# Performance work log

Hardware: AMD Instinct MI355X
Metric: run time of the kernel (lower is better)

## Reference

```python
import jax, jax.numpy as jnp
import numpy as np

B, L, D, H = 2, 2048, 1024, 16
hd = D // H
SCALE = hd ** -0.5
K = 3


def _dwconv(x_bcl, w, b):
    # x_bcl: [B, C, L]; w: [C, 1, K] depthwise; b: [C]
    y = jax.lax.conv_general_dilated(
        x_bcl, w, window_strides=(1,), padding=[((K - 1) // 2, (K - 1) // 2)],
        feature_group_count=x_bcl.shape[1],
        dimension_numbers=('NCH', 'OIH', 'NCH'))
    return y + b[None, :, None]


def setup_inputs() -> dict:
    key = jax.random.key(0)
    ks = jax.random.split(key, 11)
    def n(k, shape, s=0.02):
        return jax.random.normal(k, shape, dtype=jnp.float32) * s
    return {
        'x': jax.random.normal(ks[0], (B, L, D), dtype=jnp.float32),
        'wq': n(ks[1], (D, D)), 'wk': n(ks[2], (D, D)),
        'wv': n(ks[3], (D, D)), 'wo': n(ks[4], (D, D)),
        'cq_w': n(ks[5], (D, 1, K), 0.3), 'cq_b': n(ks[6], (D,)),
        'ck_w': n(ks[7], (D, 1, K), 0.3), 'ck_b': n(ks[8], (D,)),
        'cv_w': n(ks[9], (D, 1, K), 0.3), 'cv_b': n(ks[10], (D,)),
    }


def reference(x, wq, wk, wv, wo, cq_w, cq_b, ck_w, ck_b, cv_w, cv_b):
    # Linear projections (torch Linear: y = x @ W^T); note k scaled BEFORE conv
    q = jnp.einsum('bld,ed->ble', x, wq)
    k = jnp.einsum('bld,ed->ble', x, wk) * SCALE
    v = jnp.einsum('bld,ed->ble', x, wv)
    # Depthwise conv along sequence dim
    q = _dwconv(q.transpose(0, 2, 1), cq_w, cq_b).transpose(0, 2, 1)
    k = _dwconv(k.transpose(0, 2, 1), ck_w, ck_b).transpose(0, 2, 1)
    v = _dwconv(v.transpose(0, 2, 1), cv_w, cv_b).transpose(0, 2, 1)
    # Split heads -> [B, H, L, hd]
    q = q.reshape(B, L, H, hd).transpose(0, 2, 1, 3)
    k = k.reshape(B, L, H, hd).transpose(0, 2, 1, 3)
    v = v.reshape(B, L, H, hd).transpose(0, 2, 1, 3)
    sim = jnp.einsum('bhqd,bhkd->bhqk', q, k)
    causal = jnp.triu(jnp.ones((L, L), dtype=bool), k=1)
    sim = jnp.where(causal[None, None], -jnp.inf, sim)
    attn = jax.nn.softmax(sim, axis=-1)
    ctxt = jnp.einsum('bhqk,bhkd->bhqd', attn, v)
    out = ctxt.transpose(0, 2, 1, 3).reshape(B, L, D)
    out = jnp.einsum('bld,ed->ble', out, wo)
    return out, attn
```

## Files before the change

kernel.cpp:

```cpp
#include <hip/hip_runtime.h>
#include <hip/hip_bf16.h>


constexpr int B = 2, L = 2048, D = 1024, H = 16, HD = 64;
constexpr float SCALE = 0.125f;
constexpr int M_ROWS = B * L;

typedef short sh8 __attribute__((ext_vector_type(8)));
typedef float f32x4 __attribute__((ext_vector_type(4)));

__device__ __forceinline__ unsigned short f2bf(float f) {
  union { float f; unsigned u; } x; x.f = f;
  unsigned r = x.u + 0x7FFFu + ((x.u >> 16) & 1u);
  return (unsigned short)(r >> 16);
}
__device__ __forceinline__ float bf2f(unsigned short u) {
  union { unsigned u; float f; } x; x.u = ((unsigned)u) << 16;
  return x.f;
}

#define GLL16(gsrc, ldsbase)                                                  \
  __builtin_amdgcn_global_load_lds(                                           \
      (const __attribute__((address_space(1))) void*)(gsrc),                  \
      (__attribute__((address_space(3))) void*)(ldsbase), 16, 0, 0)

__global__ __launch_bounds__(256) void cast_x_bf16(const float* __restrict__ in,
                                                   unsigned short* __restrict__ out) {
  const size_t g = (size_t)blockIdx.x * 256 + threadIdx.x;
  const float4 a = *(const float4*)&in[g * 8];
  const float4 b = *(const float4*)&in[g * 8 + 4];
  ushort4 o0, o1;
  o0.x = f2bf(a.x); o0.y = f2bf(a.y); o0.z = f2bf(a.z); o0.w = f2bf(a.w);
  o1.x = f2bf(b.x); o1.y = f2bf(b.y); o1.z = f2bf(b.z); o1.w = f2bf(b.w);
  *(ushort4*)&out[g * 8] = o0;
  *(ushort4*)&out[g * 8 + 4] = o1;
}

__global__ __launch_bounds__(256) void cast_w4_bf16(
    const float* __restrict__ wq, const float* __restrict__ wk,
    const float* __restrict__ wv, const float* __restrict__ wo,
    unsigned short* __restrict__ out) {
  const int z = blockIdx.z;
  const float* src = (z == 0) ? wq : (z == 1) ? wk : (z == 2) ? wv : wo;
  unsigned short* dst = out + (size_t)z * 1024 * 1024;
  const size_t g = (size_t)blockIdx.x * 256 + threadIdx.x;
  const float4 a = *(const float4*)&src[g * 8];
  const float4 b = *(const float4*)&src[g * 8 + 4];
  ushort4 o0, o1;
  o0.x = f2bf(a.x); o0.y = f2bf(a.y); o0.z = f2bf(a.z); o0.w = f2bf(a.w);
  o1.x = f2bf(b.x); o1.y = f2bf(b.y); o1.z = f2bf(b.z); o1.w = f2bf(b.w);
  *(ushort4*)&dst[g * 8] = o0;
  *(ushort4*)&dst[g * 8 + 4] = o1;
}

template <bool BF16OUT>
__device__ __forceinline__ void gemm_lds_body(
    const unsigned short* __restrict__ A, const unsigned short* __restrict__ W,
    void* __restrict__ Y, float alpha) {
  __shared__ __align__(16) unsigned short As[128 * 64];
  __shared__ __align__(16) unsigned short Ws[128 * 64];
  const int tid = threadIdx.x;
  const int wave = tid >> 6, lane = tid & 63;
  const int m = lane & 15, kg = lane >> 4;
  const int m0 = blockIdx.y * 128, n0 = blockIdx.x * 128;
  const int wr = wave >> 1, wc = wave & 1;
  const int srow = lane >> 3;
  const int schunk = lane & 7;

  f32x4 acc[4][4];
#pragma unroll
  for (int i = 0; i < 4; ++i)
#pragma unroll
    for (int j = 0; j < 4; ++j) acc[i][j] = (f32x4){0.f, 0.f, 0.f, 0.f};

  for (int k0 = 0; k0 < 1024; k0 += 64) {
#pragma unroll
    for (int c = 0; c < 4; ++c) {
      const int grp = wave * 4 + c;
      const int row = grp * 8 + srow;
      GLL16(A + (size_t)(m0 + row) * 1024 + k0 + schunk * 8,
            (char*)As + grp * 1024);
      GLL16(W + (size_t)(n0 + row) * 1024 + k0 + schunk * 8,
            (char*)Ws + grp * 1024);
    }
    __syncthreads();
    sh8 af[4][2], bfr[4][2];
#pragma unroll
    for (int i = 0; i < 4; ++i)
#pragma unroll
      for (int s = 0; s < 2; ++s) {
        af[i][s] = *(const sh8*)&As[(wr * 64 + i * 16 + m) * 64 + s * 32 + kg * 8];
        bfr[i][s] = *(const sh8*)&Ws[(wc * 64 + i * 16 + m) * 64 + s * 32 + kg * 8];
      }
#pragma unroll
    for (int s = 0; s < 2; ++s)
#pragma unroll
      for (int i = 0; i < 4; ++i)
#pragma unroll
        for (int j = 0; j < 4; ++j)
          acc[i][j] = __builtin_amdgcn_mfma_f32_16x16x32_bf16(af[i][s], bfr[j][s],
                                                             acc[i][j], 0, 0, 0);
    __syncthreads();
  }

  const int R = m0 + wr * 64, C = n0 + wc * 64;
#pragma unroll
  for (int i = 0; i < 4; ++i)
#pragma unroll
    for (int j = 0; j < 4; ++j)
#pragma unroll
      for (int reg = 0; reg < 4; ++reg) {
        const int row = R + i * 16 + kg * 4 + reg;
        const int col = C + j * 16 + m;
        const float v = acc[i][j][reg] * alpha;
        if constexpr (BF16OUT)
          ((unsigned short*)Y)[(size_t)row * 1024 + col] = f2bf(v);
        else
          ((float*)Y)[(size_t)row * 1024 + col] = v;
      }
}

__global__ __launch_bounds__(256) void proj_mfma(
    const unsigned short* __restrict__ xb, const unsigned short* __restrict__ wb4,
    unsigned short* __restrict__ qpre, unsigned short* __restrict__ kpre,
    unsigned short* __restrict__ vpre) {
  const int z = blockIdx.z;
  const unsigned short* W = wb4 + (size_t)z * 1024 * 1024;
  unsigned short* Yo = (z == 0) ? qpre : (z == 1) ? kpre : vpre;
  gemm_lds_body<true>(xb, W, Yo, (z == 1) ? SCALE : 1.0f);
}

__global__ __launch_bounds__(256) void outproj_mfma(
    const unsigned short* __restrict__ ctxtb, const unsigned short* __restrict__ wob,
    float* __restrict__ out) {
  gemm_lds_body<false>(ctxtb, wob, out, 1.0f);
}

__global__ __launch_bounds__(256) void dwconv_bf16(const unsigned short* __restrict__ in,
                                                   const float* __restrict__ w,
                                                   const float* __restrict__ bias,
                                                   unsigned short* __restrict__ out) {
  const int gid = blockIdx.x * 256 + threadIdx.x;
  const int d4 = gid % (D / 4);
  const int l = (gid / (D / 4)) % L;
  const int b = gid / ((D / 4) * L);
  const int d = d4 * 4;
  const size_t base = ((size_t)b * L + l) * D + d;
  const ushort4 cu = *(const ushort4*)&in[base];
  ushort4 pu = make_ushort4(0, 0, 0, 0), nu = make_ushort4(0, 0, 0, 0);
  if (l > 0) pu = *(const ushort4*)&in[base - D];
  if (l < L - 1) nu = *(const ushort4*)&in[base + D];
  float o0 = w[(d + 0) * 3 + 0] * bf2f(pu.x) + w[(d + 0) * 3 + 1] * bf2f(cu.x) + w[(d + 0) * 3 + 2] * bf2f(nu.x) + bias[d + 0];
  float o1 = w[(d + 1) * 3 + 0] * bf2f(pu.y) + w[(d + 1) * 3 + 1] * bf2f(cu.y) + w[(d + 1) * 3 + 2] * bf2f(nu.y) + bias[d + 1];
  float o2 = w[(d + 2) * 3 + 0] * bf2f(pu.z) + w[(d + 2) * 3 + 1] * bf2f(cu.z) + w[(d + 2) * 3 + 2] * bf2f(nu.z) + bias[d + 2];
  float o3 = w[(d + 3) * 3 + 0] * bf2f(pu.w) + w[(d + 3) * 3 + 1] * bf2f(cu.w) + w[(d + 3) * 3 + 2] * bf2f(nu.w) + bias[d + 3];
  ushort4 o;
  o.x = f2bf(o0); o.y = f2bf(o1); o.z = f2bf(o2); o.w = f2bf(o3);
  *(ushort4*)&out[base] = o;
}

__global__ __launch_bounds__(256) void dwconv_v_t(const unsigned short* __restrict__ in,
                                                  const float* __restrict__ w,
                                                  const float* __restrict__ bias,
                                                  unsigned short* __restrict__ vt) {
  const int l0 = blockIdx.x * 64;
  const int h = blockIdx.y, b = blockIdx.z;
  const int d0 = h * HD;
  __shared__ unsigned short T[64][72];
  const int tid = threadIdx.x;
  const int dq = (tid & 15) * 4, lr = tid >> 4;
#pragma unroll
  for (int pass = 0; pass < 4; ++pass) {
    const int l = l0 + pass * 16 + lr;
    const size_t base = ((size_t)b * L + l) * D + d0 + dq;
    const ushort4 cu = *(const ushort4*)&in[base];
    ushort4 pu = make_ushort4(0, 0, 0, 0), nu = make_ushort4(0, 0, 0, 0);
    if (l > 0) pu = *(const ushort4*)&in[base - D];
    if (l < L - 1) nu = *(const ushort4*)&in[base + D];
    const float c[4] = {bf2f(cu.x), bf2f(cu.y), bf2f(cu.z), bf2f(cu.w)};
    const float pp[4] = {bf2f(pu.x), bf2f(pu.y), bf2f(pu.z), bf2f(pu.w)};
    const float nn[4] = {bf2f(nu.x), bf2f(nu.y), bf2f(nu.z), bf2f(nu.w)};
#pragma unroll
    for (int j = 0; j < 4; ++j) {
      const int d = d0 + dq + j;
      float o = w[d * 3 + 0] * pp[j] + w[d * 3 + 1] * c[j] + w[d * 3 + 2] * nn[j] + bias[d];
      T[dq + j][pass * 16 + lr] = f2bf(o);
    }
  }
  __syncthreads();
  const int dd = tid >> 2, lq = (tid & 3) * 16;
  const size_t rbase = ((size_t)(b * H + h) * HD + dd) * L + l0 + lq;
#pragma unroll
  for (int i = 0; i < 16; i += 4) {
    ushort4 o;
    o.x = T[dd][lq + i + 0]; o.y = T[dd][lq + i + 1];
    o.z = T[dd][lq + i + 2]; o.w = T[dd][lq + i + 3];
    *(ushort4*)&vt[rbase + i] = o;
  }
}

__global__ __launch_bounds__(256) void flash_pv(
    const unsigned short* __restrict__ qb, const unsigned short* __restrict__ kb,
    const unsigned short* __restrict__ vt, float* __restrict__ linv_g,
    unsigned short* __restrict__ ctxtb) {
  const int p = blockIdx.x, h = blockIdx.y, b = blockIdx.z;
  const int tid = threadIdx.x;
  const int wave = tid >> 6, lane = tid & 63;
  const int m = lane & 15, kg = lane >> 4;

  __shared__ unsigned short P_sh[4][16 * 72];

  const size_t bh = (size_t)b * H + h;
  const unsigned short* qbase = qb + (size_t)b * L * D + h * HD;
  const unsigned short* kbase = kb + (size_t)b * L * D + h * HD;
  const unsigned short* vbase = vt + bh * HD * L;
  float* lbase = linv_g + bh * L;

  for (int which = 0; which < 2; ++which) {
    const int qt = which ? (31 - p) : p;
    const int q0 = qt * 64;
    const int r0 = q0 + wave * 16;
    const int crow = kg * 4;

    sh8 qf[2];
#pragma unroll
    for (int s = 0; s < 2; ++s)
      qf[s] = *(const sh8*)(qbase + (size_t)(r0 + m) * D + s * 32 + kg * 8);

    f32x4 cacc[4];
#pragma unroll
    for (int ct = 0; ct < 4; ++ct) cacc[ct] = (f32x4){0.f, 0.f, 0.f, 0.f};
    float lsum[4] = {0.f, 0.f, 0.f, 0.f};

    for (int kt = 0; kt <= qt; ++kt) {
      const int kcol0 = kt * 64;
#pragma unroll
      for (int ct = 0; ct < 4; ++ct) {
        f32x4 sacc = {0.f, 0.f, 0.f, 0.f};
#pragma unroll
        for (int s = 0; s < 2; ++s) {
          sh8 kf = *(const sh8*)(kbase + (size_t)(kcol0 + ct * 16 + m) * D + s * 32 + kg * 8);
          sacc = __builtin_amdgcn_mfma_f32_16x16x32_bf16(qf[s], kf, sacc, 0, 0, 0);
        }
        const int col = kcol0 + ct * 16 + m;
#pragma unroll
        for (int reg = 0; reg < 4; ++reg) {
          const int row = r0 + crow + reg;
          const float e = (col <= row) ? __expf(sacc[reg]) : 0.f;
          lsum[reg] += e;
          P_sh[wave][(crow + reg) * 72 + ct * 16 + m] = f2bf(e);
        }
      }
      sh8 pf[2];
#pragma unroll
      for (int s = 0; s < 2; ++s)
        pf[s] = *(const sh8*)&P_sh[wave][m * 72 + s * 32 + kg * 8];
#pragma unroll
      for (int ct = 0; ct < 4; ++ct) {
#pragma unroll
        for (int s = 0; s < 2; ++s) {
          sh8 vf = *(const sh8*)(vbase + (size_t)(ct * 16 + m) * L + kcol0 + s * 32 + kg * 8);
          cacc[ct] = __builtin_amdgcn_mfma_f32_16x16x32_bf16(pf[s], vf, cacc[ct], 0, 0, 0);
        }
      }
    }

    float linv[4];
#pragma unroll
    for (int reg = 0; reg < 4; ++reg) {
      float v = lsum[reg];
      v += __shfl_xor(v, 1); v += __shfl_xor(v, 2);
      v += __shfl_xor(v, 4); v += __shfl_xor(v, 8);
      linv[reg] = 1.0f / v;
    }

#pragma unroll
    for (int ct = 0; ct < 4; ++ct)
#pragma unroll
      for (int reg = 0; reg < 4; ++reg)
        ctxtb[(size_t)(b * L + r0 + crow + reg) * D + h * HD + ct * 16 + m] =
            f2bf(cacc[ct][reg] * linv[reg]);

    if (m == 0) {
#pragma unroll
      for (int reg = 0; reg < 4; ++reg) lbase[r0 + crow + reg] = linv[reg];
    }
  }
}

__global__ __launch_bounds__(256) void attn_write(
    const unsigned short* __restrict__ qb, const unsigned short* __restrict__ kb,
    const float* __restrict__ linv_g, float* __restrict__ attn) {
  const int tc = blockIdx.x, tr = blockIdx.y, bhz = blockIdx.z;
  const int b = bhz >> 4, h = bhz & 15;
  float* attnb = attn + (size_t)bhz * L * L;

  if (tc > tr) {
    const int t = threadIdx.x;
    const int r = tr * 128 + (t >> 1);
    float* rp = attnb + (size_t)r * L + tc * 128 + (t & 1) * 64;
    const float4 z4 = make_float4(0, 0, 0, 0);
#pragma unroll
    for (int i = 0; i < 16; ++i) *(float4*)&rp[i * 4] = z4;
    return;
  }

  const int tid = threadIdx.x;
  const int wave = tid >> 6, lane = tid & 63;
  const int m = lane & 15, kg = lane >> 4;
  const int wr = wave >> 1, wc = wave & 1;
  const unsigned short* qbase = qb + (size_t)b * L * D + h * HD;
  const unsigned short* kbase = kb + (size_t)b * L * D + h * HD;
  const float* lbase = linv_g + (size_t)bhz * L;
  const int row0 = tr * 128 + wr * 64, col0 = tc * 128 + wc * 64;

  sh8 qf[4][2];
#pragma unroll
  for (int i = 0; i < 4; ++i)
#pragma unroll
    for (int s = 0; s < 2; ++s)
      qf[i][s] = *(const sh8*)(qbase + (size_t)(row0 + i * 16 + m) * D + s * 32 + kg * 8);

  f32x4 acc[4][4];
#pragma unroll
  for (int i = 0; i < 4; ++i)
#pragma unroll
    for (int j = 0; j < 4; ++j) acc[i][j] = (f32x4){0.f, 0.f, 0.f, 0.f};

#pragma unroll
  for (int s = 0; s < 2; ++s)
#pragma unroll
    for (int j = 0; j < 4; ++j) {
      sh8 kf = *(const sh8*)(kbase + (size_t)(col0 + j * 16 + m) * D + s * 32 + kg * 8);
#pragma unroll
      for (int i = 0; i < 4; ++i)
        acc[i][j] = __builtin_amdgcn_mfma_f32_16x16x32_bf16(qf[i][s], kf, acc[i][j], 0, 0, 0);
    }

  const bool diag = (tc == tr);
#pragma unroll
  for (int i = 0; i < 4; ++i)
#pragma unroll
    for (int reg = 0; reg < 4; ++reg) {
      const int row = row0 + i * 16 + kg * 4 + reg;
      const float li = lbase[row];
      float* rowp = attnb + (size_t)row * L;
#pragma unroll
      for (int j = 0; j < 4; ++j) {
        const int col = col0 + j * 16 + m;
        float val = __expf(acc[i][j][reg]) * li;
        if (diag && col > row) val = 0.f;
        rowp[col] = val;
      }
    }
}

extern "C" void kernel_launch(void* const* d_in, const int* in_sizes, int n_in,
                              void* d_out, int out_size, void* d_ws, size_t ws_size,
                              hipStream_t stream) {
  const float* x    = (const float*)d_in[0];
  const float* wq   = (const float*)d_in[1];
  const float* wk   = (const float*)d_in[2];
  const float* wv   = (const float*)d_in[3];
  const float* wo   = (const float*)d_in[4];
  const float* cq_w = (const float*)d_in[5];
  const float* cq_b = (const float*)d_in[6];
  const float* ck_w = (const float*)d_in[7];
  const float* ck_b = (const float*)d_in[8];
  const float* cv_w = (const float*)d_in[9];
  const float* cv_b = (const float*)d_in[10];

  float* out  = (float*)d_out;
  float* attn = (float*)d_out + (size_t)B * L * D;

  const size_t bufN = (size_t)B * L * D;
  unsigned short* ws16 = (unsigned short*)d_ws;
  unsigned short* qpre  = ws16 + 0 * bufN;
  unsigned short* kpre  = ws16 + 1 * bufN;
  unsigned short* vpre  = ws16 + 2 * bufN;
  unsigned short* qb    = ws16 + 3 * bufN;
  unsigned short* kbb   = ws16 + 4 * bufN;
  unsigned short* vtb   = ws16 + 5 * bufN;
  unsigned short* ctxtb = ws16 + 6 * bufN;
  unsigned short* xb    = ws16 + 7 * bufN;
  unsigned short* wb4   = ws16 + 8 * bufN;
  float* linv_g = (float*)(ws16 + 9 * bufN);

  cast_x_bf16<<<2048, 256, 0, stream>>>(x, xb);
  cast_w4_bf16<<<dim3(512, 1, 4), 256, 0, stream>>>(wq, wk, wv, wo, wb4);
  proj_mfma<<<dim3(1024 / 128, M_ROWS / 128, 3), 256, 0, stream>>>(
      xb, wb4, qpre, kpre, vpre);
  const int convBlocks = (B * L * (D / 4)) / 256;
  dwconv_bf16<<<convBlocks, 256, 0, stream>>>(qpre, cq_w, cq_b, qb);
  dwconv_bf16<<<convBlocks, 256, 0, stream>>>(kpre, ck_w, ck_b, kbb);
  dwconv_v_t<<<dim3(L / 64, H, B), 256, 0, stream>>>(vpre, cv_w, cv_b, vtb);
  flash_pv<<<dim3(16, H, B), 256, 0, stream>>>(qb, kbb, vtb, linv_g, ctxtb);
  attn_write<<<dim3(16, 16, B * H), 256, 0, stream>>>(qb, kbb, linv_g, attn);
  outproj_mfma<<<dim3(1024 / 128, M_ROWS / 128, 1), 256, 0, stream>>>(
      ctxtb, wb4 + 3ull * 1024 * 1024, out);
}
```

Before: 843.1 us.

## Split flash_pv key loop across two wave groups and swizzle GEMM LDS tiles

flash_pv now launches 512 threads per block. Two halves of waves each process alternating key tiles and combine their partial context and row sums through shared memory before normalising. The aim is to double the wave parallelism of an attention kernel that uses only 512 blocks. Separately, the projection GEMM XOR-swizzles the LDS chunk placement to reduce bank conflicts on fragment reads. The change adds an LDS reduction, extra barriers and higher LDS use per block.

Result: no change. 833.7 us (-1.1%).

```diff
diff --git a/kernel.cpp b/kernel.cpp
--- a/kernel.cpp
+++ b/kernel.cpp
@@ -73,25 +73,30 @@
 #pragma unroll
     for (int j = 0; j < 4; ++j) acc[i][j] = (f32x4){0.f, 0.f, 0.f, 0.f};
 
+  const int sch = (schunk ^ srow) * 8;
+
   for (int k0 = 0; k0 < 1024; k0 += 64) {
 #pragma unroll
     for (int c = 0; c < 4; ++c) {
       const int grp = wave * 4 + c;
       const int row = grp * 8 + srow;
-      GLL16(A + (size_t)(m0 + row) * 1024 + k0 + schunk * 8,
-            (char*)As + grp * 1024);
-      GLL16(W + (size_t)(n0 + row) * 1024 + k0 + schunk * 8,
-            (char*)Ws + grp * 1024);
+      GLL16(A + (size_t)(m0 + row) * 1024 + k0 + sch, (char*)As + grp * 1024);
+      GLL16(W + (size_t)(n0 + row) * 1024 + k0 + sch, (char*)Ws + grp * 1024);
     }
     __syncthreads();
     sh8 af[4][2], bfr[4][2];
 #pragma unroll
-    for (int i = 0; i < 4; ++i)
+    for (int i = 0; i < 4; ++i) {
+      const int ra = wr * 64 + i * 16 + m;
+      const int rb = wc * 64 + i * 16 + m;
+      const int x7 = m & 7;
 #pragma unroll
       for (int s = 0; s < 2; ++s) {
-        af[i][s] = *(const sh8*)&As[(wr * 64 + i * 16 + m) * 64 + s * 32 + kg * 8];
-        bfr[i][s] = *(const sh8*)&Ws[(wc * 64 + i * 16 + m) * 64 + s * 32 + kg * 8];
-      }
+        const int ch = ((s * 4 + kg) ^ x7) * 8;
+        af[i][s]  = *(const sh8*)&As[ra * 64 + ch];
+        bfr[i][s] = *(const sh8*)&Ws[rb * 64 + ch];
+      }
+    }
 #pragma unroll
     for (int s = 0; s < 2; ++s)
 #pragma unroll
@@ -199,16 +204,19 @@
   }
 }
 
-__global__ __launch_bounds__(256) void flash_pv(
+__global__ __launch_bounds__(512) void flash_pv(
     const unsigned short* __restrict__ qb, const unsigned short* __restrict__ kb,
     const unsigned short* __restrict__ vt, float* __restrict__ linv_g,
     unsigned short* __restrict__ ctxtb) {
   const int p = blockIdx.x, h = blockIdx.y, b = blockIdx.z;
   const int tid = threadIdx.x;
   const int wave = tid >> 6, lane = tid & 63;
+  const int wg = wave & 3, half = wave >> 2;
   const int m = lane & 15, kg = lane >> 4;
 
-  __shared__ unsigned short P_sh[4][16 * 72];
+  __shared__ unsigned short P_sh[8][16 * 72];
+  __shared__ float cpart[64 * 68];
+  __shared__ float lpart[64];
 
   const size_t bh = (size_t)b * H + h;
   const unsigned short* qbase = qb + (size_t)b * L * D + h * HD;
@@ -219,7 +227,7 @@
   for (int which = 0; which < 2; ++which) {
     const int qt = which ? (31 - p) : p;
     const int q0 = qt * 64;
-    const int r0 = q0 + wave * 16;
+    const int r0 = q0 + wg * 16;
     const int crow = kg * 4;
 
     sh8 qf[2];
@@ -232,7 +240,7 @@
     for (int ct = 0; ct < 4; ++ct) cacc[ct] = (f32x4){0.f, 0.f, 0.f, 0.f};
     float lsum[4] = {0.f, 0.f, 0.f, 0.f};
 
-    for (int kt = 0; kt <= qt; ++kt) {
+    for (int kt = half; kt <= qt; kt += 2) {
       const int kcol0 = kt * 64;
 #pragma unroll
       for (int ct = 0; ct < 4; ++ct) {
@@ -265,26 +273,45 @@
       }
     }
 
-    float linv[4];
 #pragma unroll
     for (int reg = 0; reg < 4; ++reg) {
       float v = lsum[reg];
       v += __shfl_xor(v, 1); v += __shfl_xor(v, 2);
       v += __shfl_xor(v, 4); v += __shfl_xor(v, 8);
-      linv[reg] = 1.0f / v;
-    }
-
-#pragma unroll
-    for (int ct = 0; ct < 4; ++ct)
+      lsum[reg] = v;
+    }
+
+    if (half == 1) {
+      if (m == 0) {
+#pragma unroll
+        for (int reg = 0; reg < 4; ++reg) lpart[wg * 16 + crow + reg] = lsum[reg];
+      }
+#pragma unroll
+      for (int ct = 0; ct < 4; ++ct)
+#pragma unroll
+        for (int reg = 0; reg < 4; ++reg)
+          cpart[(wg * 16 + crow + reg) * 68 + ct * 16 + m] = cacc[ct][reg];
+    }
+    __syncthreads();
+    if (half == 0) {
+      float linv[4];
 #pragma unroll
       for (int reg = 0; reg < 4; ++reg)
-        ctxtb[(size_t)(b * L + r0 + crow + reg) * D + h * HD + ct * 16 + m] =
-            f2bf(cacc[ct][reg] * linv[reg]);
-
-    if (m == 0) {
-#pragma unroll
-      for (int reg = 0; reg < 4; ++reg) lbase[r0 + crow + reg] = linv[reg];
-    }
+        linv[reg] = 1.0f / (lsum[reg] + lpart[wg * 16 + crow + reg]);
+#pragma unroll
+      for (int ct = 0; ct < 4; ++ct)
+#pragma unroll
+        for (int reg = 0; reg < 4; ++reg) {
+          const float v = cacc[ct][reg] + cpart[(wg * 16 + crow + reg) * 68 + ct * 16 + m];
+          ctxtb[(size_t)(b * L + r0 + crow + reg) * D + h * HD + ct * 16 + m] =
+              f2bf(v * linv[reg]);
+        }
+      if (m == 0) {
+#pragma unroll
+        for (int reg = 0; reg < 4; ++reg) lbase[r0 + crow + reg] = linv[reg];
+      }
+    }
+    __syncthreads();
   }
 }
 
@@ -394,7 +421,7 @@
   dwconv_bf16<<<convBlocks, 256, 0, stream>>>(qpre, cq_w, cq_b, qb);
   dwconv_bf16<<<convBlocks, 256, 0, stream>>>(kpre, ck_w, ck_b, kbb);
   dwconv_v_t<<<dim3(L / 64, H, B), 256, 0, stream>>>(vpre, cv_w, cv_b, vtb);
-  flash_pv<<<dim3(16, H, B), 256, 0, stream>>>(qb, kbb, vtb, linv_g, ctxtb);
+  flash_pv<<<dim3(16, H, B), 512, 0, stream>>>(qb, kbb, vtb, linv_g, ctxtb);
   attn_write<<<dim3(16, 16, B * H), 256, 0, stream>>>(qb, kbb, linv_g, attn);
   outproj_mfma<<<dim3(1024 / 128, M_ROWS / 128, 1), 256, 0, stream>>>(
       ctxtb, wb4 + 3ull * 1024 * 1024, out);
```
